# Kernel optimization log

Measured on AMD Instinct MI355X. Metric: run time of the kernel, lower is better.

Reference implementation:

```python
import jax, jax.numpy as jnp
import numpy as np

N = 100000      # nodes
E = 1600000     # edges
F_IN = 128
HID = 64
N_CLS = 40


def setup_inputs() -> dict:
    key = jax.random.key(0)
    ks = jax.random.split(key, 8)
    x = jax.random.normal(ks[0], (N, F_IN), dtype=jnp.float32)
    edge_index = jax.random.randint(ks[1], (2, E), 0, N, dtype=jnp.int64)
    # SAGEConv params: lin_l (applied to mean-aggregated neighbors, with bias),
    # lin_r (applied to root/self features, no bias). Glorot-ish init scaling.
    W1_l = jax.random.normal(ks[2], (F_IN, HID), dtype=jnp.float32) / np.sqrt(F_IN)
    b1 = jnp.zeros((HID,), dtype=jnp.float32)
    W1_r = jax.random.normal(ks[3], (F_IN, HID), dtype=jnp.float32) / np.sqrt(F_IN)
    W2_l = jax.random.normal(ks[4], (HID, N_CLS), dtype=jnp.float32) / np.sqrt(HID)
    b2 = jnp.zeros((N_CLS,), dtype=jnp.float32)
    W2_r = jax.random.normal(ks[5], (HID, N_CLS), dtype=jnp.float32) / np.sqrt(HID)
    return {"x": x, "edge_index": edge_index,
            "W1_l": W1_l, "b1": b1, "W1_r": W1_r,
            "W2_l": W2_l, "b2": b2, "W2_r": W2_r}


def _sage_conv(x, src, dst, W_l, b_l, W_r):
    # mean aggregation of neighbor features: messages flow src -> dst
    msgs = x[src]                                              # [E, d]
    summed = jax.ops.segment_sum(msgs, dst, num_segments=N)    # [N, d]
    cnt = jax.ops.segment_sum(jnp.ones((src.shape[0],), x.dtype), dst,
                              num_segments=N)                  # [N]
    agg = summed / jnp.maximum(cnt, 1.0)[:, None]
    return agg @ W_l + b_l + x @ W_r


def reference(x, edge_index, W1_l, b1, W1_r, W2_l, b2, W2_r):
    src, dst = edge_index[0], edge_index[1]
    h = jax.nn.relu(_sage_conv(x, src, dst, W1_l, b1, W1_r))
    # dropout: identity in eval mode
    logits = _sage_conv(h, src, dst, W2_l, b2, W2_r)
    return jax.nn.log_softmax(logits, axis=1)
```

## Files before the change

### kernel.cpp

```cpp
#include <hip/hip_runtime.h>
#include <math.h>

#define N_NODES 100000
#define F_IN    128
#define HID     64
#define N_CLS   40
#define MT      (N_NODES / 16)

#define BSHIFT  9
#define BSZ     512
#define NB      ((N_NODES + BSZ - 1) / BSZ)
#define EPB     4096

typedef __attribute__((ext_vector_type(8))) short bf8_t;
typedef __attribute__((ext_vector_type(4))) float f4_t;
typedef __attribute__((ext_vector_type(2))) float f2v_t;

typedef unsigned short ushort_t;
typedef unsigned int uint_t;
typedef unsigned char uchar_t;

__device__ __forceinline__ ushort_t f2b(float f) {
    union { float f; uint_t u; } c; c.f = f;
    uint_t u = c.u + 0x7FFFu + ((c.u >> 16) & 1u);
    return (ushort_t)(u >> 16);
}
__device__ __forceinline__ float b2f(ushort_t h) {
    union { uint_t u; float f; } c; c.u = ((uint_t)h) << 16;
    return c.f;
}

#if defined(__has_builtin)
#if __has_builtin(__builtin_amdgcn_cvt_pk_f32_fp8) && __has_builtin(__builtin_amdgcn_cvt_pk_fp8_f32)
#define HAVE_FP8_HW 1
#endif
#endif

__device__ __forceinline__ uchar_t fp8_enc(float v) {
#ifdef HAVE_FP8_HW
    return (uchar_t)(__builtin_amdgcn_cvt_pk_fp8_f32(v, v, 0, false) & 0xff);
#else
    union { float f; uint_t u; } c; c.f = v;
    uint_t s = c.u >> 31;
    float av = fabsf(v);
    if (av > 448.f) av = 448.f;
    int e;
    float m = frexpf(av, &e);
    int ee = e + 6;
    uchar_t r;
    if (av == 0.f) r = 0;
    else if (ee <= 0) {
        int q = (int)(av * 512.f + 0.5f);
        if (q > 7) q = 7;
        r = (uchar_t)q;
    } else {
        int q = (int)(m * 16.f + 0.5f);
        if (q == 16) { q = 8; ee += 1; }
        if (ee > 15) { ee = 15; q = 15; }
        r = (uchar_t)((ee << 3) | (q & 7));
    }
    return r | (uchar_t)(s << 7);
#endif
}

__device__ __forceinline__ f2v_t fp8x2_dec_lo(uint_t w) {
#ifdef HAVE_FP8_HW
    return __builtin_amdgcn_cvt_pk_f32_fp8(w, false);
#else
    f2v_t r;
    for (int k = 0; k < 2; ++k) {
        uchar_t b = (w >> (8 * k)) & 0xff;
        uint_t s = (b >> 7) & 1, e = (b >> 3) & 15, m = b & 7;
        float f;
        if (e) { union { uint_t u; float ff; } c;
                 c.u = (s << 31) | ((e + 120) << 23) | (m << 20); f = c.ff; }
        else   { f = (float)m * 0.001953125f; if (s) f = -f; }
        r[k] = f;
    }
    return r;
#endif
}
__device__ __forceinline__ f2v_t fp8x2_dec_hi(uint_t w) {
#ifdef HAVE_FP8_HW
    return __builtin_amdgcn_cvt_pk_f32_fp8(w, true);
#else
    return fp8x2_dec_lo(w >> 16);
#endif
}

__global__ void block_hist_kernel(const int* __restrict__ ei, int E,
                                  int* __restrict__ blockHist) {
    __shared__ int cnt[NB];
    int t = threadIdx.x, blk = blockIdx.x;
    for (int i = t; i < NB; i += 256) cnt[i] = 0;
    __syncthreads();
    int e0 = blk * EPB;
#pragma unroll
    for (int i = 0; i < EPB / 256; ++i) {
        int e = e0 + i * 256 + t;
        if (e < E) atomicAdd(&cnt[ei[E + e] >> BSHIFT], 1);
    }
    __syncthreads();
    for (int i = t; i < NB; i += 256) blockHist[blk * NB + i] = cnt[i];
}

__global__ void col_scan_kernel(const int* __restrict__ blockHist, int nblk,
                                int* __restrict__ blockBase,
                                int* __restrict__ btot) {
    __shared__ int ss[256];
    __shared__ int carry;
    int bin = blockIdx.x, t = threadIdx.x;
    if (t == 0) carry = 0;
    __syncthreads();
    for (int c0 = 0; c0 < nblk; c0 += 256) {
        int b = c0 + t;
        int v = (b < nblk) ? blockHist[b * NB + bin] : 0;
        ss[t] = v;
        __syncthreads();
        for (int off = 1; off < 256; off <<= 1) {
            int u = (t >= off) ? ss[t - off] : 0;
            __syncthreads();
            ss[t] += u;
            __syncthreads();
        }
        if (b < nblk) blockBase[b * NB + bin] = carry + ss[t] - v;
        __syncthreads();
        if (t == 255) carry += ss[255];
        __syncthreads();
    }
    if (t == 0) btot[bin] = carry;
}

__global__ void scatter_pairs_kernel(const int* __restrict__ ei, int E,
                                     const int* __restrict__ blockBase,
                                     const int* __restrict__ btot,
                                     uint_t* __restrict__ pairs) {
    __shared__ int cur[NB];
    __shared__ int base[NB];
    __shared__ int ss[256];
    int t = threadIdx.x, blk = blockIdx.x;
    int v = (t < NB) ? btot[t] : 0;
    ss[t] = v;
    __syncthreads();
    for (int off = 1; off < 256; off <<= 1) {
        int u = (t >= off) ? ss[t - off] : 0;
        __syncthreads();
        ss[t] += u;
        __syncthreads();
    }
    if (t < NB) {
        cur[t] = 0;
        base[t] = (ss[t] - v) + blockBase[blk * NB + t];
    }
    __syncthreads();
    int e0 = blk * EPB;
#pragma unroll
    for (int i = 0; i < EPB / 256; ++i) {
        int e = e0 + i * 256 + t;
        if (e < E) {
            int src = ei[e];
            int dst = ei[E + e];
            int bin = dst >> BSHIFT;
            int r = atomicAdd(&cur[bin], 1);
            pairs[base[bin] + r] = ((uint_t)src << BSHIFT) | (uint_t)(dst & (BSZ - 1));
        }
    }
}

__global__ void bucket_sort_kernel(const uint_t* __restrict__ pairs,
                                   const int* __restrict__ btot,
                                   int* __restrict__ rowptr,
                                   int* __restrict__ csr) {
    __shared__ int hist[BSZ];
    __shared__ int lofs[BSZ];
    int bin = blockIdx.x, t = threadIdx.x;
    int pv = (t < NB) ? btot[t] : 0;
    lofs[t] = pv;
    __syncthreads();
    for (int off = 1; off < BSZ; off <<= 1) {
        int u = (t >= off) ? lofs[t - off] : 0;
        __syncthreads();
        lofs[t] += u;
        __syncthreads();
    }
    int base = (bin > 0) ? lofs[bin - 1] : 0;
    int cnt = btot[bin];
    __syncthreads();
    hist[t] = 0;
    __syncthreads();
    for (int i = t; i < cnt; i += BSZ)
        atomicAdd(&hist[pairs[base + i] & (BSZ - 1)], 1);
    __syncthreads();
    int v = hist[t];
    lofs[t] = v;
    __syncthreads();
    for (int off = 1; off < BSZ; off <<= 1) {
        int u = (t >= off) ? lofs[t - off] : 0;
        __syncthreads();
        lofs[t] += u;
        __syncthreads();
    }
    int excl = lofs[t] - v;
    int d_global = (bin << BSHIFT) + t;
    if (d_global < N_NODES) rowptr[d_global] = base + excl;
    if (bin == NB - 1 && t == 0) rowptr[N_NODES] = base + cnt;
    __syncthreads();
    lofs[t] = excl;
    hist[t] = 0;
    __syncthreads();
    for (int i = t; i < cnt; i += BSZ) {
        uint_t p = pairs[base + i];
        int lb = p & (BSZ - 1);
        int r = atomicAdd(&hist[lb], 1);
        csr[base + lofs[lb] + r] = (int)(p >> BSHIFT);
    }
}

__global__ void cvt_w_kernel(const float* __restrict__ W1l,
                             const float* __restrict__ W1r,
                             const float* __restrict__ W2l,
                             const float* __restrict__ W2r,
                             ushort_t* __restrict__ W1t,
                             ushort_t* __restrict__ W2t) {
    int t = blockIdx.x * blockDim.x + threadIdx.x;
    if (t < 128 * F_IN) {
        int n = t / F_IN, k = t - n * F_IN;
        float v = (n < HID) ? W1l[k * HID + n] : W1r[k * HID + (n - HID)];
        W1t[t] = f2b(v);
    } else if (t < 128 * F_IN + 80 * HID) {
        int u = t - 128 * F_IN;
        int n = u / HID, k = u - n * HID;
        float v = (n < N_CLS) ? W2l[k * N_CLS + n] : W2r[k * N_CLS + (n - N_CLS)];
        W2t[u] = f2b(v);
    }
}

__global__ void gemm1_mfma_kernel(const float* __restrict__ x,
                                  const ushort_t* __restrict__ W1t,
                                  uchar_t* __restrict__ y1a,
                                  uchar_t* __restrict__ y1b,
                                  ushort_t* __restrict__ z1b) {
    __shared__ uchar_t sy[64][80];
    __shared__ ushort_t sz[64][72];
    int tid = threadIdx.x;
    int wave = tid >> 6, lane = tid & 63;
    int tile = blockIdx.x * 4 + wave;
    int m0b = blockIdx.x * 64;
    if (tile < MT) {
        int m0 = tile * 16;
        int r = lane & 15, q = lane >> 4;
        const float* xr = x + (size_t)(m0 + r) * F_IN + q * 8;
        bf8_t a[4];
#pragma unroll
        for (int kt = 0; kt < 4; ++kt) {
            float4 u = *(const float4*)(xr + kt * 32);
            float4 v = *(const float4*)(xr + kt * 32 + 4);
            bf8_t tt;
            tt[0] = (short)f2b(u.x); tt[1] = (short)f2b(u.y);
            tt[2] = (short)f2b(u.z); tt[3] = (short)f2b(u.w);
            tt[4] = (short)f2b(v.x); tt[5] = (short)f2b(v.y);
            tt[6] = (short)f2b(v.z); tt[7] = (short)f2b(v.w);
            a[kt] = tt;
        }
        int lr0 = wave * 16 + q * 4;
#pragma unroll
        for (int tn = 0; tn < 8; ++tn) {
            const ushort_t* wr = W1t + (size_t)(tn * 16 + r) * F_IN + q * 8;
            f4_t acc = {0.f, 0.f, 0.f, 0.f};
#pragma unroll
            for (int kt = 0; kt < 4; ++kt) {
                bf8_t b = *(const bf8_t*)(wr + kt * 32);
                acc = __builtin_amdgcn_mfma_f32_16x16x32_bf16(a[kt], b, acc, 0, 0, 0);
            }
            int col = tn * 16 + r;
            if (col < 64) {
#pragma unroll
                for (int rr = 0; rr < 4; ++rr)
                    sy[lr0 + rr][col] = fp8_enc(acc[rr]);
            } else {
#pragma unroll
                for (int rr = 0; rr < 4; ++rr)
                    sz[lr0 + rr][col - 64] = f2b(acc[rr]);
            }
        }
    }
    __syncthreads();
    int vrows = N_NODES - m0b; if (vrows > 64) vrows = 64;
    for (int idx = tid; idx < vrows * 2; idx += 256) {
        int row = idx >> 1, c = (idx & 1) << 4;
        *(uint4*)(y1a + (size_t)(m0b + row) * 32 + c) = *(const uint4*)&sy[row][c];
        *(uint4*)(y1b + (size_t)(m0b + row) * 32 + c) = *(const uint4*)&sy[row][c + 32];
    }
    for (int idx = tid; idx < vrows * 8; idx += 256) {
        int row = idx >> 3, c = (idx & 7) << 3;
        *(uint4*)(z1b + (size_t)(m0b + row) * HID + c) = *(const uint4*)&sz[row][c];
    }
}

__global__ void agg1_half_kernel(const int* __restrict__ rowptr,
                                 const int* __restrict__ csr,
                                 const uchar_t* __restrict__ y1h,
                                 const ushort_t* __restrict__ z1b,
                                 const float* __restrict__ b1,
                                 ushort_t* __restrict__ hb, int half) {
    int gid = blockIdx.x * blockDim.x + threadIdx.x;
    int wave = gid >> 6, lane = gid & 63;
    int g = lane >> 3, l = lane & 7;
    int n = wave * 8 + g;
    if (n >= N_NODES) return;
    int beg = rowptr[n], end = rowptr[n + 1];
    float a0 = 0.f, a1 = 0.f, a2 = 0.f, a3 = 0.f;
    int i = beg;
    for (; i + 3 < end; i += 4) {
        int s0 = csr[i], s1 = csr[i + 1], s2 = csr[i + 2], s3 = csr[i + 3];
        uint_t w0 = *(const uint_t*)(y1h + (size_t)s0 * 32 + l * 4);
        uint_t w1 = *(const uint_t*)(y1h + (size_t)s1 * 32 + l * 4);
        uint_t w2 = *(const uint_t*)(y1h + (size_t)s2 * 32 + l * 4);
        uint_t w3 = *(const uint_t*)(y1h + (size_t)s3 * 32 + l * 4);
        f2v_t p0 = fp8x2_dec_lo(w0), p1 = fp8x2_dec_hi(w0);
        f2v_t q0 = fp8x2_dec_lo(w1), q1 = fp8x2_dec_hi(w1);
        f2v_t r0 = fp8x2_dec_lo(w2), r1 = fp8x2_dec_hi(w2);
        f2v_t t0 = fp8x2_dec_lo(w3), t1 = fp8x2_dec_hi(w3);
        a0 += (p0[0] + q0[0]) + (r0[0] + t0[0]);
        a1 += (p0[1] + q0[1]) + (r0[1] + t0[1]);
        a2 += (p1[0] + q1[0]) + (r1[0] + t1[0]);
        a3 += (p1[1] + q1[1]) + (r1[1] + t1[1]);
    }
    for (; i < end; ++i) {
        uint_t w = *(const uint_t*)(y1h + (size_t)csr[i] * 32 + l * 4);
        f2v_t p0 = fp8x2_dec_lo(w), p1 = fp8x2_dec_hi(w);
        a0 += p0[0]; a1 += p0[1]; a2 += p1[0]; a3 += p1[1];
    }
    float inv = 1.0f / fmaxf((float)(end - beg), 1.0f);
    int c = half * 32 + l * 4;
    float4 bb = *(const float4*)(b1 + c);
    ushort4 zz = *(const ushort4*)(z1b + (size_t)n * HID + c);
    float r0 = fmaxf(fmaf(a0, inv, bb.x + b2f(zz.x)), 0.f);
    float r1 = fmaxf(fmaf(a1, inv, bb.y + b2f(zz.y)), 0.f);
    float r2 = fmaxf(fmaf(a2, inv, bb.z + b2f(zz.z)), 0.f);
    float r3 = fmaxf(fmaf(a3, inv, bb.w + b2f(zz.w)), 0.f);
    ushort4 o;
    o.x = f2b(r0); o.y = f2b(r1); o.z = f2b(r2); o.w = f2b(r3);
    *(ushort4*)(hb + (size_t)n * HID + c) = o;
}

__global__ void gemm2_mfma_kernel(const ushort_t* __restrict__ hb,
                                  const ushort_t* __restrict__ W2t,
                                  uchar_t* __restrict__ y2f8,
                                  ushort_t* __restrict__ z2b) {
    __shared__ uchar_t sy2[64 * 40];
    __shared__ ushort_t sz2[64][56];
    int tid = threadIdx.x;
    int wave = tid >> 6, lane = tid & 63;
    int tile = blockIdx.x * 4 + wave;
    int m0b = blockIdx.x * 64;
    if (tile < MT) {
        int m0 = tile * 16;
        int r = lane & 15, q = lane >> 4;
        const ushort_t* hr = hb + (size_t)(m0 + r) * HID + q * 8;
        bf8_t a[2];
#pragma unroll
        for (int kt = 0; kt < 2; ++kt)
            a[kt] = *(const bf8_t*)(hr + kt * 32);
        int lr0 = wave * 16 + q * 4;
#pragma unroll
        for (int tn = 0; tn < 5; ++tn) {
            const ushort_t* wr = W2t + (size_t)(tn * 16 + r) * HID + q * 8;
            f4_t acc = {0.f, 0.f, 0.f, 0.f};
#pragma unroll
            for (int kt = 0; kt < 2; ++kt) {
                bf8_t b = *(const bf8_t*)(wr + kt * 32);
                acc = __builtin_amdgcn_mfma_f32_16x16x32_bf16(a[kt], b, acc, 0, 0, 0);
            }
            int col = tn * 16 + r;
            if (col < N_CLS) {
#pragma unroll
                for (int rr = 0; rr < 4; ++rr)
                    sy2[(lr0 + rr) * 40 + col] = fp8_enc(acc[rr]);
            } else {
#pragma unroll
                for (int rr = 0; rr < 4; ++rr)
                    sz2[lr0 + rr][col - N_CLS] = f2b(acc[rr]);
            }
        }
    }
    __syncthreads();
    int vrows = N_NODES - m0b; if (vrows > 64) vrows = 64;
    int nch = (vrows * 40) >> 4;
    for (int idx = tid; idx < nch; idx += 256)
        *(uint4*)(y2f8 + (size_t)m0b * 40 + idx * 16) = *(const uint4*)&sy2[idx * 16];
    for (int idx = tid; idx < vrows * 5; idx += 256) {
        int row = idx / 5, c = (idx - row * 5) * 8;
        *(uint4*)(z2b + (size_t)(m0b + row) * HID + c) = *(const uint4*)&sz2[row][c];
    }
}

__global__ void agg2_kernel(const int* __restrict__ rowptr,
                            const int* __restrict__ csr,
                            const uchar_t* __restrict__ y2f8,
                            const ushort_t* __restrict__ z2b,
                            const float* __restrict__ b2,
                            float* __restrict__ out) {
    int gid = blockIdx.x * blockDim.x + threadIdx.x;
    int wave = gid >> 6, lane = gid & 63;
    int g = lane >> 4, l = lane & 15;
    int n = wave * 4 + g;
    if (n >= N_NODES) return;
    int beg = rowptr[n], end = rowptr[n + 1];
    float a0 = 0.f, a1 = 0.f, a2 = 0.f, a3 = 0.f;
    float4 bb = make_float4(0.f, 0.f, 0.f, 0.f);
    ushort4 zz; zz.x = 0; zz.y = 0; zz.z = 0; zz.w = 0;
    int c0 = l * 4;
    if (l < 10) {
        int i = beg;
        for (; i + 3 < end; i += 4) {
            int s0 = csr[i], s1 = csr[i + 1], s2 = csr[i + 2], s3 = csr[i + 3];
            uint_t w0 = *(const uint_t*)(y2f8 + (size_t)s0 * 40 + c0);
            uint_t w1 = *(const uint_t*)(y2f8 + (size_t)s1 * 40 + c0);
            uint_t w2 = *(const uint_t*)(y2f8 + (size_t)s2 * 40 + c0);
            uint_t w3 = *(const uint_t*)(y2f8 + (size_t)s3 * 40 + c0);
            f2v_t p0 = fp8x2_dec_lo(w0), p1 = fp8x2_dec_hi(w0);
            f2v_t q0 = fp8x2_dec_lo(w1), q1 = fp8x2_dec_hi(w1);
            f2v_t r0 = fp8x2_dec_lo(w2), r1 = fp8x2_dec_hi(w2);
            f2v_t t0 = fp8x2_dec_lo(w3), t1 = fp8x2_dec_hi(w3);
            a0 += (p0[0] + q0[0]) + (r0[0] + t0[0]);
            a1 += (p0[1] + q0[1]) + (r0[1] + t0[1]);
            a2 += (p1[0] + q1[0]) + (r1[0] + t1[0]);
            a3 += (p1[1] + q1[1]) + (r1[1] + t1[1]);
        }
        for (; i < end; ++i) {
            uint_t w = *(const uint_t*)(y2f8 + (size_t)csr[i] * 40 + c0);
            f2v_t p0 = fp8x2_dec_lo(w), p1 = fp8x2_dec_hi(w);
            a0 += p0[0]; a1 += p0[1]; a2 += p1[0]; a3 += p1[1];
        }
        bb = *(const float4*)(b2 + c0);
        zz = *(const ushort4*)(z2b + (size_t)n * HID + c0);
    }
    float inv = 1.0f / fmaxf((float)(end - beg), 1.0f);
    float v0 = (c0 + 0 < N_CLS) ? fmaf(a0, inv, bb.x + b2f(zz.x)) : -INFINITY;
    float v1 = (c0 + 1 < N_CLS) ? fmaf(a1, inv, bb.y + b2f(zz.y)) : -INFINITY;
    float v2 = (c0 + 2 < N_CLS) ? fmaf(a2, inv, bb.z + b2f(zz.z)) : -INFINITY;
    float v3 = (c0 + 3 < N_CLS) ? fmaf(a3, inv, bb.w + b2f(zz.w)) : -INFINITY;

    float m = fmaxf(fmaxf(v0, v1), fmaxf(v2, v3));
#pragma unroll
    for (int off = 1; off < 16; off <<= 1)
        m = fmaxf(m, __shfl_xor(m, off, 64));
    float s = 0.f;
    if (v0 > -INFINITY) s += expf(v0 - m);
    if (v1 > -INFINITY) s += expf(v1 - m);
    if (v2 > -INFINITY) s += expf(v2 - m);
    if (v3 > -INFINITY) s += expf(v3 - m);
#pragma unroll
    for (int off = 1; off < 16; off <<= 1)
        s += __shfl_xor(s, off, 64);
    float ls = logf(s);
    if (l < 10) {
        float4 o = make_float4(v0 - m - ls, v1 - m - ls, v2 - m - ls, v3 - m - ls);
        *(float4*)(out + (size_t)n * N_CLS + c0) = o;
    }
}

extern "C" void kernel_launch(void* const* d_in, const int* in_sizes, int n_in,
                              void* d_out, int out_size, void* d_ws, size_t ws_size,
                              hipStream_t stream) {
    const float* x   = (const float*)d_in[0];
    const int*   ei  = (const int*)d_in[1];
    const float* W1l = (const float*)d_in[2];
    const float* b1  = (const float*)d_in[3];
    const float* W1r = (const float*)d_in[4];
    const float* W2l = (const float*)d_in[5];
    const float* b2  = (const float*)d_in[6];
    const float* W2r = (const float*)d_in[7];
    float* out = (float*)d_out;
    const int E = in_sizes[1] / 2;
    const int nblk = (E + EPB - 1) / EPB;

    char* p = (char*)d_ws;
    auto take = [&](size_t bytes) {
        char* q = p;
        p += (bytes + 15) & ~(size_t)15;
        return (void*)q;
    };
    int* rowptr     = (int*)take(sizeof(int) * (N_NODES + 4));
    int* blockHist  = (int*)take(sizeof(int) * (size_t)nblk * NB);
    int* blockBase  = (int*)take(sizeof(int) * (size_t)nblk * NB);
    int* btot       = (int*)take(sizeof(int) * NB);
    uint_t* pairs   = (uint_t*)take(sizeof(uint_t) * (size_t)E);
    int* csr        = (int*)take(sizeof(int) * (size_t)E);
    ushort_t* W1t   = (ushort_t*)take(sizeof(ushort_t) * 128 * F_IN);
    ushort_t* W2t   = (ushort_t*)take(sizeof(ushort_t) * 80 * HID);
    uchar_t* y1a    = (uchar_t*)take(sizeof(uchar_t) * (size_t)N_NODES * 32);
    uchar_t* y1b    = (uchar_t*)take(sizeof(uchar_t) * (size_t)N_NODES * 32);
    ushort_t* z1b   = (ushort_t*)take(sizeof(ushort_t) * (size_t)N_NODES * HID);
    ushort_t* hb    = (ushort_t*)take(sizeof(ushort_t) * (size_t)N_NODES * HID);
    uchar_t* y2f8 = y1a;
    ushort_t* z2b = z1b;

    const int B = 256;

    block_hist_kernel<<<nblk, 256, 0, stream>>>(ei, E, blockHist);
    col_scan_kernel<<<NB, 256, 0, stream>>>(blockHist, nblk, blockBase, btot);
    scatter_pairs_kernel<<<nblk, 256, 0, stream>>>(ei, E, blockBase, btot, pairs);
    bucket_sort_kernel<<<NB, BSZ, 0, stream>>>(pairs, btot, rowptr, csr);

    cvt_w_kernel<<<(128 * F_IN + 80 * HID + B - 1) / B, B, 0, stream>>>(
        W1l, W1r, W2l, W2r, W1t, W2t);

    int gemm_blocks = (MT + 3) / 4;
    int t_agg1 = (N_NODES / 8) * 64;
    int t_agg2 = (N_NODES / 4) * 64;

    gemm1_mfma_kernel<<<gemm_blocks, B, 0, stream>>>(x, W1t, y1a, y1b, z1b);
    agg1_half_kernel<<<(t_agg1 + B - 1) / B, B, 0, stream>>>(rowptr, csr, y1a, z1b, b1, hb, 0);
    agg1_half_kernel<<<(t_agg1 + B - 1) / B, B, 0, stream>>>(rowptr, csr, y1b, z1b, b1, hb, 1);
    gemm2_mfma_kernel<<<gemm_blocks, B, 0, stream>>>(hb, W2t, y2f8, z2b);
    agg2_kernel<<<(t_agg2 + B - 1) / B, B, 0, stream>>>(rowptr, csr, y2f8, z2b, b2, out);
}
```

Measured before the change: 259.6 us.

## Merge split-half layer-1 aggregation into one pass with 16-byte gathers

Layer-1 fp8 neighbor features move from two 32-byte half tables to one 64-byte row. The two half-aggregation launches become a single kernel where 4 lanes per node each gather 16 bytes, so the CSR list is read once instead of twice. The agg2 gather loop is also unrolled to 8 neighbors to keep more loads in flight. The cost is more registers per thread and a larger gathered footprint per pass, which the earlier half split was presumably meant to keep cache-resident.

```diff
diff --git a/kernel.cpp b/kernel.cpp
--- a/kernel.cpp
+++ b/kernel.cpp
@@ -237,8 +237,7 @@
 
 __global__ void gemm1_mfma_kernel(const float* __restrict__ x,
                                   const ushort_t* __restrict__ W1t,
-                                  uchar_t* __restrict__ y1a,
-                                  uchar_t* __restrict__ y1b,
+                                  uchar_t* __restrict__ y1f8,
                                   ushort_t* __restrict__ z1b) {
     __shared__ uchar_t sy[64][80];
     __shared__ ushort_t sz[64][72];
@@ -286,10 +285,9 @@
     }
     __syncthreads();
     int vrows = N_NODES - m0b; if (vrows > 64) vrows = 64;
-    for (int idx = tid; idx < vrows * 2; idx += 256) {
-        int row = idx >> 1, c = (idx & 1) << 4;
-        *(uint4*)(y1a + (size_t)(m0b + row) * 32 + c) = *(const uint4*)&sy[row][c];
-        *(uint4*)(y1b + (size_t)(m0b + row) * 32 + c) = *(const uint4*)&sy[row][c + 32];
+    for (int idx = tid; idx < vrows * 4; idx += 256) {
+        int row = idx >> 2, c = (idx & 3) << 4;
+        *(uint4*)(y1f8 + (size_t)(m0b + row) * 64 + c) = *(const uint4*)&sy[row][c];
     }
     for (int idx = tid; idx < vrows * 8; idx += 256) {
         int row = idx >> 3, c = (idx & 7) << 3;
@@ -297,51 +295,65 @@
     }
 }
 
-__global__ void agg1_half_kernel(const int* __restrict__ rowptr,
-                                 const int* __restrict__ csr,
-                                 const uchar_t* __restrict__ y1h,
-                                 const ushort_t* __restrict__ z1b,
-                                 const float* __restrict__ b1,
-                                 ushort_t* __restrict__ hb, int half) {
+__device__ __forceinline__ void acc16(float* acc, uint4 v) {
+    f2v_t p;
+    p = fp8x2_dec_lo(v.x); acc[0]  += p[0]; acc[1]  += p[1];
+    p = fp8x2_dec_hi(v.x); acc[2]  += p[0]; acc[3]  += p[1];
+    p = fp8x2_dec_lo(v.y); acc[4]  += p[0]; acc[5]  += p[1];
+    p = fp8x2_dec_hi(v.y); acc[6]  += p[0]; acc[7]  += p[1];
+    p = fp8x2_dec_lo(v.z); acc[8]  += p[0]; acc[9]  += p[1];
+    p = fp8x2_dec_hi(v.z); acc[10] += p[0]; acc[11] += p[1];
+    p = fp8x2_dec_lo(v.w); acc[12] += p[0]; acc[13] += p[1];
+    p = fp8x2_dec_hi(v.w); acc[14] += p[0]; acc[15] += p[1];
+}
+
+__global__ void agg1_kernel(const int* __restrict__ rowptr,
+                            const int* __restrict__ csr,
+                            const uchar_t* __restrict__ y1f8,
+                            const ushort_t* __restrict__ z1b,
+                            const float* __restrict__ b1,
+                            ushort_t* __restrict__ hb) {
     int gid = blockIdx.x * blockDim.x + threadIdx.x;
     int wave = gid >> 6, lane = gid & 63;
-    int g = lane >> 3, l = lane & 7;
-    int n = wave * 8 + g;
+    int g = lane >> 2, l = lane & 3;
+    int n = wave * 16 + g;
     if (n >= N_NODES) return;
     int beg = rowptr[n], end = rowptr[n + 1];
-    float a0 = 0.f, a1 = 0.f, a2 = 0.f, a3 = 0.f;
+    float acc[16];
+#pragma unroll
+    for (int j = 0; j < 16; ++j) acc[j] = 0.f;
+    const uchar_t* yb = y1f8 + l * 16;
     int i = beg;
     for (; i + 3 < end; i += 4) {
         int s0 = csr[i], s1 = csr[i + 1], s2 = csr[i + 2], s3 = csr[i + 3];
-        uint_t w0 = *(const uint_t*)(y1h + (size_t)s0 * 32 + l * 4);
-        uint_t w1 = *(const uint_t*)(y1h + (size_t)s1 * 32 + l * 4);
-        uint_t w2 = *(const uint_t*)(y1h + (size_t)s2 * 32 + l * 4);
-        uint_t w3 = *(const uint_t*)(y1h + (size_t)s3 * 32 + l * 4);
-        f2v_t p0 = fp8x2_dec_lo(w0), p1 = fp8x2_dec_hi(w0);
-        f2v_t q0 = fp8x2_dec_lo(w1), q1 = fp8x2_dec_hi(w1);
-        f2v_t r0 = fp8x2_dec_lo(w2), r1 = fp8x2_dec_hi(w2);
-        f2v_t t0 = fp8x2_dec_lo(w3), t1 = fp8x2_dec_hi(w3);
-        a0 += (p0[0] + q0[0]) + (r0[0] + t0[0]);
-        a1 += (p0[1] + q0[1]) + (r0[1] + t0[1]);
-        a2 += (p1[0] + q1[0]) + (r1[0] + t1[0]);
-        a3 += (p1[1] + q1[1]) + (r1[1] + t1[1]);
+        uint4 w0 = *(const uint4*)(yb + (size_t)s0 * 64);
+        uint4 w1 = *(const uint4*)(yb + (size_t)s1 * 64);
+        uint4 w2 = *(const uint4*)(yb + (size_t)s2 * 64);
+        uint4 w3 = *(const uint4*)(yb + (size_t)s3 * 64);
+        acc16(acc, w0); acc16(acc, w1); acc16(acc, w2); acc16(acc, w3);
     }
     for (; i < end; ++i) {
-        uint_t w = *(const uint_t*)(y1h + (size_t)csr[i] * 32 + l * 4);
-        f2v_t p0 = fp8x2_dec_lo(w), p1 = fp8x2_dec_hi(w);
-        a0 += p0[0]; a1 += p0[1]; a2 += p1[0]; a3 += p1[1];
+        uint4 w = *(const uint4*)(yb + (size_t)csr[i] * 64);
+        acc16(acc, w);
     }
     float inv = 1.0f / fmaxf((float)(end - beg), 1.0f);
-    int c = half * 32 + l * 4;
-    float4 bb = *(const float4*)(b1 + c);
-    ushort4 zz = *(const ushort4*)(z1b + (size_t)n * HID + c);
-    float r0 = fmaxf(fmaf(a0, inv, bb.x + b2f(zz.x)), 0.f);
-    float r1 = fmaxf(fmaf(a1, inv, bb.y + b2f(zz.y)), 0.f);
-    float r2 = fmaxf(fmaf(a2, inv, bb.z + b2f(zz.z)), 0.f);
-    float r3 = fmaxf(fmaf(a3, inv, bb.w + b2f(zz.w)), 0.f);
-    ushort4 o;
-    o.x = f2b(r0); o.y = f2b(r1); o.z = f2b(r2); o.w = f2b(r3);
-    *(ushort4*)(hb + (size_t)n * HID + c) = o;
+    int c = l * 16;
+    ushort_t zz[16];
+    *(uint4*)&zz[0] = *(const uint4*)(z1b + (size_t)n * HID + c);
+    *(uint4*)&zz[8] = *(const uint4*)(z1b + (size_t)n * HID + c + 8);
+    float bv[16];
+    *(float4*)&bv[0]  = *(const float4*)(b1 + c);
+    *(float4*)&bv[4]  = *(const float4*)(b1 + c + 4);
+    *(float4*)&bv[8]  = *(const float4*)(b1 + c + 8);
+    *(float4*)&bv[12] = *(const float4*)(b1 + c + 12);
+    ushort_t o[16];
+#pragma unroll
+    for (int j = 0; j < 16; ++j) {
+        float r = fmaxf(fmaf(acc[j], inv, bv[j] + b2f(zz[j])), 0.f);
+        o[j] = f2b(r);
+    }
+    *(uint4*)(hb + (size_t)n * HID + c)     = *(const uint4*)&o[0];
+    *(uint4*)(hb + (size_t)n * HID + c + 8) = *(const uint4*)&o[8];
 }
 
 __global__ void gemm2_mfma_kernel(const ushort_t* __restrict__ hb,
@@ -413,20 +425,50 @@
     int c0 = l * 4;
     if (l < 10) {
         int i = beg;
+        for (; i + 7 < end; i += 8) {
+            int s0 = csr[i],     s1 = csr[i + 1], s2 = csr[i + 2], s3 = csr[i + 3];
+            int s4 = csr[i + 4], s5 = csr[i + 5], s6 = csr[i + 6], s7 = csr[i + 7];
+            uint_t w0 = *(const uint_t*)(y2f8 + (size_t)s0 * 40 + c0);
+            uint_t w1 = *(const uint_t*)(y2f8 + (size_t)s1 * 40 + c0);
+            uint_t w2 = *(const uint_t*)(y2f8 + (size_t)s2 * 40 + c0);
+            uint_t w3 = *(const uint_t*)(y2f8 + (size_t)s3 * 40 + c0);
+            uint_t w4 = *(const uint_t*)(y2f8 + (size_t)s4 * 40 + c0);
+            uint_t w5 = *(const uint_t*)(y2f8 + (size_t)s5 * 40 + c0);
+            uint_t w6 = *(const uint_t*)(y2f8 + (size_t)s6 * 40 + c0);
+            uint_t w7 = *(const uint_t*)(y2f8 + (size_t)s7 * 40 + c0);
+            f2v_t p;
+            p = fp8x2_dec_lo(w0); a0 += p[0]; a1 += p[1];
+            p = fp8x2_dec_hi(w0); a2 += p[0]; a3 += p[1];
+            p = fp8x2_dec_lo(w1); a0 += p[0]; a1 += p[1];
+            p = fp8x2_dec_hi(w1); a2 += p[0]; a3 += p[1];
+            p = fp8x2_dec_lo(w2); a0 += p[0]; a1 += p[1];
+            p = fp8x2_dec_hi(w2); a2 += p[0]; a3 += p[1];
+            p = fp8x2_dec_lo(w3); a0 += p[0]; a1 += p[1];
+            p = fp8x2_dec_hi(w3); a2 += p[0]; a3 += p[1];
+            p = fp8x2_dec_lo(w4); a0 += p[0]; a1 += p[1];
+            p = fp8x2_dec_hi(w4); a2 += p[0]; a3 += p[1];
+            p = fp8x2_dec_lo(w5); a0 += p[0]; a1 += p[1];
+            p = fp8x2_dec_hi(w5); a2 += p[0]; a3 += p[1];
+            p = fp8x2_dec_lo(w6); a0 += p[0]; a1 += p[1];
+            p = fp8x2_dec_hi(w6); a2 += p[0]; a3 += p[1];
+            p = fp8x2_dec_lo(w7); a0 += p[0]; a1 += p[1];
+            p = fp8x2_dec_hi(w7); a2 += p[0]; a3 += p[1];
+        }
         for (; i + 3 < end; i += 4) {
             int s0 = csr[i], s1 = csr[i + 1], s2 = csr[i + 2], s3 = csr[i + 3];
             uint_t w0 = *(const uint_t*)(y2f8 + (size_t)s0 * 40 + c0);
             uint_t w1 = *(const uint_t*)(y2f8 + (size_t)s1 * 40 + c0);
             uint_t w2 = *(const uint_t*)(y2f8 + (size_t)s2 * 40 + c0);
             uint_t w3 = *(const uint_t*)(y2f8 + (size_t)s3 * 40 + c0);
-            f2v_t p0 = fp8x2_dec_lo(w0), p1 = fp8x2_dec_hi(w0);
-            f2v_t q0 = fp8x2_dec_lo(w1), q1 = fp8x2_dec_hi(w1);
-            f2v_t r0 = fp8x2_dec_lo(w2), r1 = fp8x2_dec_hi(w2);
-            f2v_t t0 = fp8x2_dec_lo(w3), t1 = fp8x2_dec_hi(w3);
-            a0 += (p0[0] + q0[0]) + (r0[0] + t0[0]);
-            a1 += (p0[1] + q0[1]) + (r0[1] + t0[1]);
-            a2 += (p1[0] + q1[0]) + (r1[0] + t1[0]);
-            a3 += (p1[1] + q1[1]) + (r1[1] + t1[1]);
+            f2v_t p;
+            p = fp8x2_dec_lo(w0); a0 += p[0]; a1 += p[1];
+            p = fp8x2_dec_hi(w0); a2 += p[0]; a3 += p[1];
+            p = fp8x2_dec_lo(w1); a0 += p[0]; a1 += p[1];
+            p = fp8x2_dec_hi(w1); a2 += p[0]; a3 += p[1];
+            p = fp8x2_dec_lo(w2); a0 += p[0]; a1 += p[1];
+            p = fp8x2_dec_hi(w2); a2 += p[0]; a3 += p[1];
+            p = fp8x2_dec_lo(w3); a0 += p[0]; a1 += p[1];
+            p = fp8x2_dec_hi(w3); a2 += p[0]; a3 += p[1];
         }
         for (; i < end; ++i) {
             uint_t w = *(const uint_t*)(y2f8 + (size_t)csr[i] * 40 + c0);
@@ -490,11 +532,10 @@
     int* csr        = (int*)take(sizeof(int) * (size_t)E);
     ushort_t* W1t   = (ushort_t*)take(sizeof(ushort_t) * 128 * F_IN);
     ushort_t* W2t   = (ushort_t*)take(sizeof(ushort_t) * 80 * HID);
-    uchar_t* y1a    = (uchar_t*)take(sizeof(uchar_t) * (size_t)N_NODES * 32);
-    uchar_t* y1b    = (uchar_t*)take(sizeof(uchar_t) * (size_t)N_NODES * 32);
+    uchar_t* y1f8   = (uchar_t*)take(sizeof(uchar_t) * (size_t)N_NODES * 64);
     ushort_t* z1b   = (ushort_t*)take(sizeof(ushort_t) * (size_t)N_NODES * HID);
     ushort_t* hb    = (ushort_t*)take(sizeof(ushort_t) * (size_t)N_NODES * HID);
-    uchar_t* y2f8 = y1a;
+    uchar_t* y2f8 = y1f8;
     ushort_t* z2b = z1b;
 
     const int B = 256;
@@ -508,12 +549,11 @@
         W1l, W1r, W2l, W2r, W1t, W2t);
 
     int gemm_blocks = (MT + 3) / 4;
-    int t_agg1 = (N_NODES / 8) * 64;
+    int t_agg1 = (N_NODES / 16) * 64;
     int t_agg2 = (N_NODES / 4) * 64;
 
-    gemm1_mfma_kernel<<<gemm_blocks, B, 0, stream>>>(x, W1t, y1a, y1b, z1b);
-    agg1_half_kernel<<<(t_agg1 + B - 1) / B, B, 0, stream>>>(rowptr, csr, y1a, z1b, b1, hb, 0);
-    agg1_half_kernel<<<(t_agg1 + B - 1) / B, B, 0, stream>>>(rowptr, csr, y1b, z1b, b1, hb, 1);
+    gemm1_mfma_kernel<<<gemm_blocks, B, 0, stream>>>(x, W1t, y1f8, z1b);
+    agg1_kernel<<<(t_agg1 + B - 1) / B, B, 0, stream>>>(rowptr, csr, y1f8, z1b, b1, hb);
     gemm2_mfma_kernel<<<gemm_blocks, B, 0, stream>>>(hb, W2t, y2f8, z2b);
     agg2_kernel<<<(t_agg2 + B - 1) / B, B, 0, stream>>>(rowptr, csr, y2f8, z2b, b2, out);
 }
```

Result: faster. 238.7 us (-8.0%).
